# Optimization experiments

Hardware: AMD Instinct MI355X
Metric: run time of the kernel (lower is better)

## Reference

```python
import jax, jax.numpy as jnp
import numpy as np

B, S, D, F, E, K = 2, 2048, 1024, 4096, 8, 2


def setup_inputs() -> dict:
    key = jax.random.key(0)
    ks = jax.random.split(key, 6)
    s = 0.02  # init scale
    return {
        "x": jax.random.normal(ks[0], (B, S, D), dtype=jnp.float32),
        "Wr": jax.random.normal(ks[1], (D, E), dtype=jnp.float32) * s,
        "br": jnp.zeros((E,), dtype=jnp.float32),
        "W1": jax.random.normal(ks[2], (E, D, F), dtype=jnp.float32) * s,
        "b1": jnp.zeros((E, F), dtype=jnp.float32),
        "W2": jax.random.normal(ks[3], (E, F, D), dtype=jnp.float32) * s,
        "b2": jnp.zeros((E, D), dtype=jnp.float32),
        "top_k": K,
    }


def reference(x, Wr, br, W1, b1, W2, b2, top_k):
    b, s, d = x.shape
    e = Wr.shape[1]
    xt = x.reshape(-1, d)                              # [T, D], T = b*s
    logits = xt @ Wr + br                              # [T, E]
    probs = jax.nn.softmax(logits, axis=-1)            # [T, E] router probabilities
    topw, topi = jax.lax.top_k(probs, top_k)           # [T, K] each
    # combine weight per (token, expert): weight if expert in token's top-k else 0
    cw = jnp.sum(jax.nn.one_hot(topi, e, dtype=x.dtype) * topw[..., None], axis=1)  # [T, E]
    # dense grouped FFN: every expert over every token, then weighted combine
    h = jax.nn.relu(jnp.einsum('td,edf->tef', xt, W1) + b1)   # [T, E, F]
    y = jnp.einsum('tef,efd->ted', h, W2) + b2                # [T, E, D]
    out = jnp.einsum('te,ted->td', cw, y).reshape(b, s, d)    # [B, S, D]
    return out, probs.reshape(b, s, e)
```

## Files before the change

kernel.cpp:

```cpp
#include <hip/hip_runtime.h>
#include <hip/hip_bf16.h>


#define T_TOK 4096
#define D_DIM 1024
#define F_DIM 4096
#define E_NUM 8
#define CAP_ROWS 9216
#define N_TILES (CAP_ROWS/128)

typedef __attribute__((ext_vector_type(8))) short short8v;
typedef __attribute__((ext_vector_type(8))) unsigned short ushort8v;
typedef __attribute__((ext_vector_type(4))) float f32x4;

static __device__ __forceinline__ unsigned short f2bf(float f){
  union { float f; unsigned u; } v; v.f = f;
  unsigned r = (v.u + 0x7fffu + ((v.u >> 16) & 1u)) >> 16;
  return (unsigned short)r;
}
static __device__ __forceinline__ float bf2f(unsigned short s){
  union { unsigned u; float f; } v; v.u = ((unsigned)s) << 16;
  return v.f;
}

static __device__ __forceinline__ void gload16(const void* g, void* l) {
  __builtin_amdgcn_global_load_lds(
      (const __attribute__((address_space(1))) unsigned int*)g,
      (__attribute__((address_space(3))) unsigned int*)l, 16, 0, 0);
}

__global__ __launch_bounds__(256) void k_router(
    const float* __restrict__ x, const float* __restrict__ Wr,
    const float* __restrict__ br, float* __restrict__ probs_out,
    int* __restrict__ topi, float* __restrict__ topw, int* __restrict__ counts,
    unsigned short* __restrict__ xbf)
{
  const int lane = threadIdx.x & 63;
  const int t = blockIdx.x * 4 + (threadIdx.x >> 6);
  float xv[16];
  #pragma unroll
  for (int i = 0; i < 16; ++i) xv[i] = x[(size_t)t*D_DIM + i*64 + lane];
  #pragma unroll
  for (int i = 0; i < 16; ++i) xbf[(size_t)t*D_DIM + i*64 + lane] = f2bf(xv[i]);
  float pe[E_NUM];
  #pragma unroll
  for (int e = 0; e < E_NUM; ++e) {
    float p = 0.f;
    #pragma unroll
    for (int i = 0; i < 16; ++i) p += xv[i] * Wr[(i*64 + lane)*E_NUM + e];
    #pragma unroll
    for (int off = 32; off >= 1; off >>= 1) p += __shfl_xor(p, off);
    pe[e] = p + br[e];
  }
  float m = pe[0];
  #pragma unroll
  for (int e = 1; e < E_NUM; ++e) m = fmaxf(m, pe[e]);
  float s = 0.f;
  #pragma unroll
  for (int e = 0; e < E_NUM; ++e) { pe[e] = expf(pe[e] - m); s += pe[e]; }
  const float inv = 1.f / s;
  int e1 = 0; float v1 = pe[0];
  #pragma unroll
  for (int e = 1; e < E_NUM; ++e) if (pe[e] > v1) { v1 = pe[e]; e1 = e; }
  int e2 = (e1 == 0) ? 1 : 0; float v2 = pe[e2];
  #pragma unroll
  for (int e = 0; e < E_NUM; ++e) if (e != e1 && pe[e] > v2) { v2 = pe[e]; e2 = e; }
  if (lane == 0) {
    #pragma unroll
    for (int e = 0; e < E_NUM; ++e) probs_out[(size_t)t*E_NUM + e] = pe[e] * inv;
    topi[t*2+0] = e1; topw[t*2+0] = v1 * inv;
    topi[t*2+1] = e2; topw[t*2+1] = v2 * inv;
    atomicAdd(&counts[e1], 1);
    atomicAdd(&counts[e2], 1);
  }
}

__global__ __launch_bounds__(256) void k_assign(
    const int* __restrict__ counts,
    const int* __restrict__ topi, const float* __restrict__ topw,
    int* __restrict__ cursor,
    int* __restrict__ rows_token, float* __restrict__ rows_w,
    int* __restrict__ pair_of, int* __restrict__ tile_e)
{
  __shared__ int base_s[E_NUM + 1];
  if (threadIdx.x == 0) {
    int base = 0;
    #pragma unroll
    for (int e = 0; e < E_NUM; ++e) {
      base_s[e] = base;
      base += ((counts[e] + 127) >> 7) << 7;
    }
    base_s[E_NUM] = base;
  }
  __syncthreads();
  if (blockIdx.x == 0 && threadIdx.x < N_TILES) {
    const int r0 = threadIdx.x << 7;
    int e = -1;
    #pragma unroll
    for (int k = 0; k < E_NUM; ++k)
      if (r0 >= base_s[k] && r0 < base_s[k+1]) e = k;
    tile_e[threadIdx.x] = e;
  }
  const int t = blockIdx.x * 256 + threadIdx.x;
  if (t < T_TOK) {
    #pragma unroll
    for (int k = 0; k < 2; ++k) {
      const int e = topi[t*2+k];
      const int slot = atomicAdd(&cursor[e], 1);
      const int pid = base_s[e] + slot;
      rows_token[pid] = t;
      rows_w[pid] = topw[t*2+k];
      pair_of[t*2+k] = pid;
    }
  }
}

template<int R, int C>
__global__ __launch_bounds__(256) void k_tcvt(const float* __restrict__ in,
                                              unsigned short* __restrict__ out)
{
  const size_t eo = (size_t)blockIdx.z * R * C;
  const int r0 = blockIdx.y * 64, c0 = blockIdx.x * 64;
  __shared__ unsigned short ls[64][66];
  const int t = threadIdx.x;
  const int rr = t >> 4, cc = (t & 15) * 4;
  #pragma unroll
  for (int p = 0; p < 4; ++p) {
    const float4 v = *(const float4*)&in[eo + (size_t)(r0 + p*16 + rr)*C + c0 + cc];
    ls[p*16+rr][cc+0]=f2bf(v.x); ls[p*16+rr][cc+1]=f2bf(v.y);
    ls[p*16+rr][cc+2]=f2bf(v.z); ls[p*16+rr][cc+3]=f2bf(v.w);
  }
  __syncthreads();
  const int kc = (t & 7) * 8, nn0 = t >> 3;
  #pragma unroll
  for (int p = 0; p < 2; ++p) {
    const int nn = nn0 + p*32;
    ushort8v o;
    #pragma unroll
    for (int j = 0; j < 8; ++j) o[j] = ls[kc + j][nn];
    *(ushort8v*)&out[eo + (size_t)(c0 + nn)*R + r0 + kc] = o;
  }
}

template<bool GATHER, int NDIM, int KFULL, int EPI>
__global__ __launch_bounds__(256, 2) void k_gemm(
    const unsigned short* __restrict__ A,
    const unsigned short* __restrict__ Bt,
    const float* __restrict__ bias,
    const int* __restrict__ tile_e,
    const int* __restrict__ rows_token,
    const float* __restrict__ rows_w,
    unsigned short* __restrict__ outp,
    int nkt, int kch)
{
  const int tot = gridDim.x * gridDim.y;
  int flat = blockIdx.x * gridDim.y + blockIdx.y;
  flat = (flat & 7) * (tot >> 3) + (flat >> 3);
  const int bx = flat / gridDim.y;
  const int by = flat % gridDim.y;
  const int e = tile_e[by];
  if (e < 0) return;
  const int rt = by * 128;
  const int ntc = bx * 128;
  const int koff = blockIdx.z * kch;
  __shared__ __align__(16) unsigned short LB[2][256 * 64];
  const int tid = threadIdx.x;
  const int lane = tid & 63;
  const int w = tid >> 6;
  const int lr = lane >> 3;
  const int g  = (lane & 7) ^ lr;
  const unsigned short* gp[8];
  unsigned lbase[8];
  if (w < 2) {
    #pragma unroll
    for (int i = 0; i < 8; ++i) {
      const int rl = w*64 + i*8 + lr;
      const int rowidx = GATHER ? rows_token[rt + rl] : (rt + rl);
      gp[i] = A + (size_t)rowidx * KFULL + koff + g*8;
      lbase[i] = (unsigned)((w*64 + i*8) * 64);
    }
  } else {
    const unsigned short* Be = Bt + (size_t)e * NDIM * KFULL;
    #pragma unroll
    for (int i = 0; i < 8; ++i) {
      const int rl = (w-2)*64 + i*8 + lr;
      gp[i] = Be + (size_t)(ntc + rl) * KFULL + koff + g*8;
      lbase[i] = (unsigned)((128*64) + ((w-2)*64 + i*8) * 64);
    }
  }
  const int wr = w >> 1, wc = w & 1;
  const int cl = lane & 15, rgb = lane >> 4;
  const int sz = cl & 7;
  f32x4 acc[4][4] = {};

  #define STG8(tt, bb)                                          \
    { const int _ko = (tt) * 64;                                \
      _Pragma("unroll")                                         \
      for (int _i = 0; _i < 8; ++_i)                            \
        gload16(gp[_i] + _ko, &LB[bb][lbase[_i]]); }

  STG8(0, 0)
  asm volatile("s_waitcnt vmcnt(0)" ::: "memory");
  __builtin_amdgcn_s_barrier();

  for (int t = 0; t < nkt; ++t) {
    const int bb = t & 1;
    if (t + 1 < nkt) STG8(t+1, bb^1)
    const unsigned short* Sb = &LB[bb][0];
    short8v a[4][2], b[4][2];
    #pragma unroll
    for (int m = 0; m < 4; ++m) {
      a[m][0] = *(const short8v*)&Sb[(wr*64 + m*16 + cl)*64 + ((0*4+rgb)^sz)*8];
      a[m][1] = *(const short8v*)&Sb[(wr*64 + m*16 + cl)*64 + ((1*4+rgb)^sz)*8];
    }
    #pragma unroll
    for (int n = 0; n < 4; ++n) {
      b[n][0] = *(const short8v*)&Sb[(128*64) + (wc*64 + n*16 + cl)*64 + ((0*4+rgb)^sz)*8];
      b[n][1] = *(const short8v*)&Sb[(128*64) + (wc*64 + n*16 + cl)*64 + ((1*4+rgb)^sz)*8];
    }
    __builtin_amdgcn_s_setprio(1);
    #pragma unroll
    for (int m = 0; m < 4; ++m)
      #pragma unroll
      for (int n = 0; n < 4; ++n) {
        acc[m][n] = __builtin_amdgcn_mfma_f32_16x16x32_bf16(a[m][0], b[n][0], acc[m][n], 0, 0, 0);
        acc[m][n] = __builtin_amdgcn_mfma_f32_16x16x32_bf16(a[m][1], b[n][1], acc[m][n], 0, 0, 0);
      }
    __builtin_amdgcn_s_setprio(0);
    asm volatile("s_waitcnt vmcnt(0)" ::: "memory");
    __builtin_amdgcn_s_barrier();
  }
  #undef STG8

  unsigned short* op = outp;
  if (EPI == 2) op += (size_t)blockIdx.z * CAP_ROWS * NDIM;
  const bool addb = (EPI == 1) || (blockIdx.z == 0);
  const size_t ebias = (size_t)e * NDIM;
  #pragma unroll
  for (int m = 0; m < 4; ++m) {
    const int row = rt + wr*64 + m*16 + rgb*4;
    float4 rw4 = make_float4(0,0,0,0);
    if (EPI == 2) rw4 = *(const float4*)&rows_w[row];
    #pragma unroll
    for (int n = 0; n < 4; ++n) {
      const int col = ntc + wc*64 + n*16 + cl;
      const float bv = addb ? bias[ebias + col] : 0.f;
      #pragma unroll
      for (int r = 0; r < 4; ++r) {
        float v = acc[m][n][r] + bv;
        if (EPI == 1) v = fmaxf(v, 0.f);
        else          v *= ((const float*)&rw4)[r];
        const unsigned short hb = f2bf(v);
        const unsigned short ob = (unsigned short)__shfl_xor((int)(unsigned)hb, 1);
        if ((lane & 1) == 0) {
          const unsigned pk = (unsigned)hb | ((unsigned)ob << 16);
          *(unsigned*)&op[(size_t)(row + r)*NDIM + col] = pk;
        }
      }
    }
  }
}

__global__ __launch_bounds__(256) void k_combine(
    const unsigned short* __restrict__ yp, const int* __restrict__ pair_of,
    float* __restrict__ out, int ksplit)
{
  const int gid = blockIdx.x * 256 + threadIdx.x;
  const int t = gid >> 7;
  const int c = (gid & 127) * 8;
  float o[8] = {0,0,0,0,0,0,0,0};
  #pragma unroll
  for (int k = 0; k < 2; ++k) {
    const int p = pair_of[t*2+k];
    for (int s = 0; s < ksplit; ++s) {
      const ushort8v v = *(const ushort8v*)&yp[((size_t)s*CAP_ROWS + p)*D_DIM + c];
      #pragma unroll
      for (int j = 0; j < 8; ++j) o[j] += bf2f(v[j]);
    }
  }
  float4 o0; o0.x=o[0]; o0.y=o[1]; o0.z=o[2]; o0.w=o[3];
  float4 o1; o1.x=o[4]; o1.y=o[5]; o1.z=o[6]; o1.w=o[7];
  *(float4*)&out[(size_t)t*D_DIM + c]     = o0;
  *(float4*)&out[(size_t)t*D_DIM + c + 4] = o1;
}

extern "C" void kernel_launch(void* const* d_in, const int* in_sizes, int n_in,
                              void* d_out, int out_size, void* d_ws, size_t ws_size,
                              hipStream_t stream)
{
  const float* x  = (const float*)d_in[0];
  const float* Wr = (const float*)d_in[1];
  const float* br = (const float*)d_in[2];
  const float* W1 = (const float*)d_in[3];
  const float* b1 = (const float*)d_in[4];
  const float* W2 = (const float*)d_in[5];
  const float* b2 = (const float*)d_in[6];
  (void)in_sizes; (void)n_in; (void)out_size;

  float* out   = (float*)d_out;
  float* probs = out + (size_t)T_TOK * D_DIM;

  char* w = (char*)d_ws;
  size_t off = 0;
  int*   counts     = (int*)(w + off); off += 256;
  int*   cursor     = (int*)(w + off); off += 256;
  int*   rows_token = (int*)(w + off); off += (size_t)CAP_ROWS*4;
  float* rows_w     = (float*)(w + off); off += (size_t)CAP_ROWS*4;
  const size_t zbytes = off;
  int*   tile_e     = (int*)(w + off); off += 3072;
  int*   topi       = (int*)(w + off); off += (size_t)T_TOK*2*4;
  float* topw       = (float*)(w + off); off += (size_t)T_TOK*2*4;
  int*   pair_of    = (int*)(w + off); off += (size_t)T_TOK*2*4;
  off = (off + 255) & ~(size_t)255;
  unsigned short* xbf = (unsigned short*)(w + off); off += (size_t)T_TOK*D_DIM*2;
  unsigned short* Wt  = (unsigned short*)(w + off); off += (size_t)E_NUM*D_DIM*F_DIM*2;
  unsigned short* h   = (unsigned short*)(w + off); off += (size_t)CAP_ROWS*F_DIM*2;
  unsigned short* yp  = (unsigned short*)(w + off);
  const size_t ypart_bytes = (size_t)CAP_ROWS * D_DIM * 2;
  int ksplit = 1;
  if (ws_size >= off + 4 * ypart_bytes) ksplit = 4;
  else if (ws_size >= off + 2 * ypart_bytes) ksplit = 2;
  const int kch2 = F_DIM / ksplit;
  const int nkt2 = kch2 / 64;

  hipMemsetAsync(d_ws, 0, zbytes, stream);
  k_router<<<T_TOK / 4, 256, 0, stream>>>(x, Wr, br, probs, topi, topw, counts, xbf);
  k_assign<<<T_TOK / 256, 256, 0, stream>>>(counts, topi, topw, cursor,
                                            rows_token, rows_w, pair_of, tile_e);
  k_tcvt<D_DIM, F_DIM><<<dim3(F_DIM/64, D_DIM/64, E_NUM), 256, 0, stream>>>(W1, Wt);
  k_gemm<true, F_DIM, D_DIM, 1><<<dim3(F_DIM/128, N_TILES, 1), 256, 0, stream>>>(
      xbf, Wt, b1, tile_e, rows_token, rows_w, h, D_DIM/64, D_DIM);
  k_tcvt<F_DIM, D_DIM><<<dim3(D_DIM/64, F_DIM/64, E_NUM), 256, 0, stream>>>(W2, Wt);
  k_gemm<false, D_DIM, F_DIM, 2><<<dim3(D_DIM/128, N_TILES, ksplit), 256, 0, stream>>>(
      h, Wt, b2, tile_e, rows_token, rows_w, yp, nkt2, kch2);
  k_combine<<<T_TOK * D_DIM / 8 / 256, 256, 0, stream>>>(yp, pair_of, out, ksplit);
}
```

Measured before the change: 469.3 us.

## Make grouped GEMMs persistent with fixed grid and reduce FFN2 split-K to two

Both expert GEMM kernels now launch a fixed grid of 512 workgroups that loop over output tiles in an XCD-grouped order, where before there was one workgroup per tile. This skips empty capacity tiles without paying for launching them and keeps the tiles a workgroup walks through close together for L2 reuse. The second GEMM's split-K drops from up to 4 to at most 2, which cuts partial-output traffic and combine work but leaves fewer tiles to spread across the grid. The loop adds per-tile index arithmetic, and leftover tiles at the end may balance unevenly across workgroups.

```diff
diff --git a/kernel.cpp b/kernel.cpp
--- a/kernel.cpp
+++ b/kernel.cpp
@@ -8,6 +8,7 @@
 #define E_NUM 8
 #define CAP_ROWS 9216
 #define N_TILES (CAP_ROWS/128)
+#define PGRID 512
 
 typedef __attribute__((ext_vector_type(8))) short short8v;
 typedef __attribute__((ext_vector_type(8))) unsigned short ushort8v;
@@ -151,110 +152,121 @@
     const int* __restrict__ rows_token,
     const float* __restrict__ rows_w,
     unsigned short* __restrict__ outp,
-    int nkt, int kch)
-{
-  const int tot = gridDim.x * gridDim.y;
-  int flat = blockIdx.x * gridDim.y + blockIdx.y;
-  flat = (flat & 7) * (tot >> 3) + (flat >> 3);
-  const int bx = flat / gridDim.y;
-  const int by = flat % gridDim.y;
-  const int e = tile_e[by];
-  if (e < 0) return;
-  const int rt = by * 128;
-  const int ntc = bx * 128;
-  const int koff = blockIdx.z * kch;
+    int tot, int nbx, int nkt, int kch)
+{
+  const int q = blockIdx.x & 7;
+  const int bslot = blockIdx.x >> 3;
+  const int region = tot >> 3;
+  const int cpq = region / N_TILES;
   __shared__ __align__(16) unsigned short LB[2][256 * 64];
   const int tid = threadIdx.x;
   const int lane = tid & 63;
   const int w = tid >> 6;
   const int lr = lane >> 3;
   const int g  = (lane & 7) ^ lr;
-  const unsigned short* gp[8];
   unsigned lbase[8];
   if (w < 2) {
     #pragma unroll
-    for (int i = 0; i < 8; ++i) {
-      const int rl = w*64 + i*8 + lr;
-      const int rowidx = GATHER ? rows_token[rt + rl] : (rt + rl);
-      gp[i] = A + (size_t)rowidx * KFULL + koff + g*8;
-      lbase[i] = (unsigned)((w*64 + i*8) * 64);
-    }
+    for (int i = 0; i < 8; ++i) lbase[i] = (unsigned)((w*64 + i*8) * 64);
   } else {
-    const unsigned short* Be = Bt + (size_t)e * NDIM * KFULL;
-    #pragma unroll
-    for (int i = 0; i < 8; ++i) {
-      const int rl = (w-2)*64 + i*8 + lr;
-      gp[i] = Be + (size_t)(ntc + rl) * KFULL + koff + g*8;
-      lbase[i] = (unsigned)((128*64) + ((w-2)*64 + i*8) * 64);
-    }
+    #pragma unroll
+    for (int i = 0; i < 8; ++i) lbase[i] = (unsigned)((128*64) + ((w-2)*64 + i*8) * 64);
   }
   const int wr = w >> 1, wc = w & 1;
   const int cl = lane & 15, rgb = lane >> 4;
   const int sz = cl & 7;
-  f32x4 acc[4][4] = {};
-
-  #define STG8(tt, bb)                                          \
-    { const int _ko = (tt) * 64;                                \
-      _Pragma("unroll")                                         \
-      for (int _i = 0; _i < 8; ++_i)                            \
-        gload16(gp[_i] + _ko, &LB[bb][lbase[_i]]); }
-
-  STG8(0, 0)
-  asm volatile("s_waitcnt vmcnt(0)" ::: "memory");
-  __builtin_amdgcn_s_barrier();
-
-  for (int t = 0; t < nkt; ++t) {
-    const int bb = t & 1;
-    if (t + 1 < nkt) STG8(t+1, bb^1)
-    const unsigned short* Sb = &LB[bb][0];
-    short8v a[4][2], b[4][2];
-    #pragma unroll
-    for (int m = 0; m < 4; ++m) {
-      a[m][0] = *(const short8v*)&Sb[(wr*64 + m*16 + cl)*64 + ((0*4+rgb)^sz)*8];
-      a[m][1] = *(const short8v*)&Sb[(wr*64 + m*16 + cl)*64 + ((1*4+rgb)^sz)*8];
-    }
-    #pragma unroll
-    for (int n = 0; n < 4; ++n) {
-      b[n][0] = *(const short8v*)&Sb[(128*64) + (wc*64 + n*16 + cl)*64 + ((0*4+rgb)^sz)*8];
-      b[n][1] = *(const short8v*)&Sb[(128*64) + (wc*64 + n*16 + cl)*64 + ((1*4+rgb)^sz)*8];
-    }
-    __builtin_amdgcn_s_setprio(1);
-    #pragma unroll
-    for (int m = 0; m < 4; ++m)
-      #pragma unroll
-      for (int n = 0; n < 4; ++n) {
-        acc[m][n] = __builtin_amdgcn_mfma_f32_16x16x32_bf16(a[m][0], b[n][0], acc[m][n], 0, 0, 0);
-        acc[m][n] = __builtin_amdgcn_mfma_f32_16x16x32_bf16(a[m][1], b[n][1], acc[m][n], 0, 0, 0);
-      }
-    __builtin_amdgcn_s_setprio(0);
+
+  for (int tw = bslot; tw < region; tw += (PGRID >> 3)) {
+    const int combo = q * cpq + tw / N_TILES;
+    const int by = tw % N_TILES;
+    const int bx = combo % nbx;
+    const int z  = combo / nbx;
+    const int e = tile_e[by];
+    if (e < 0) continue;
+    const int rt = by * 128;
+    const int ntc = bx * 128;
+    const int koff = z * kch;
+    const unsigned short* gp[8];
+    if (w < 2) {
+      #pragma unroll
+      for (int i = 0; i < 8; ++i) {
+        const int rl = w*64 + i*8 + lr;
+        const int rowidx = GATHER ? rows_token[rt + rl] : (rt + rl);
+        gp[i] = A + (size_t)rowidx * KFULL + koff + g*8;
+      }
+    } else {
+      const unsigned short* Be = Bt + (size_t)e * NDIM * KFULL;
+      #pragma unroll
+      for (int i = 0; i < 8; ++i) {
+        const int rl = (w-2)*64 + i*8 + lr;
+        gp[i] = Be + (size_t)(ntc + rl) * KFULL + koff + g*8;
+      }
+    }
+    f32x4 acc[4][4] = {};
+
+    #define STG8(tt, bb)                                          \
+      { const int _ko = (tt) * 64;                                \
+        _Pragma("unroll")                                         \
+        for (int _i = 0; _i < 8; ++_i)                            \
+          gload16(gp[_i] + _ko, &LB[bb][lbase[_i]]); }
+
+    STG8(0, 0)
     asm volatile("s_waitcnt vmcnt(0)" ::: "memory");
     __builtin_amdgcn_s_barrier();
-  }
-  #undef STG8
-
-  unsigned short* op = outp;
-  if (EPI == 2) op += (size_t)blockIdx.z * CAP_ROWS * NDIM;
-  const bool addb = (EPI == 1) || (blockIdx.z == 0);
-  const size_t ebias = (size_t)e * NDIM;
-  #pragma unroll
-  for (int m = 0; m < 4; ++m) {
-    const int row = rt + wr*64 + m*16 + rgb*4;
-    float4 rw4 = make_float4(0,0,0,0);
-    if (EPI == 2) rw4 = *(const float4*)&rows_w[row];
-    #pragma unroll
-    for (int n = 0; n < 4; ++n) {
-      const int col = ntc + wc*64 + n*16 + cl;
-      const float bv = addb ? bias[ebias + col] : 0.f;
-      #pragma unroll
-      for (int r = 0; r < 4; ++r) {
-        float v = acc[m][n][r] + bv;
-        if (EPI == 1) v = fmaxf(v, 0.f);
-        else          v *= ((const float*)&rw4)[r];
-        const unsigned short hb = f2bf(v);
-        const unsigned short ob = (unsigned short)__shfl_xor((int)(unsigned)hb, 1);
-        if ((lane & 1) == 0) {
-          const unsigned pk = (unsigned)hb | ((unsigned)ob << 16);
-          *(unsigned*)&op[(size_t)(row + r)*NDIM + col] = pk;
+
+    for (int t = 0; t < nkt; ++t) {
+      const int bb = t & 1;
+      if (t + 1 < nkt) STG8(t+1, bb^1)
+      const unsigned short* Sb = &LB[bb][0];
+      short8v a[4][2], b[4][2];
+      #pragma unroll
+      for (int m = 0; m < 4; ++m) {
+        a[m][0] = *(const short8v*)&Sb[(wr*64 + m*16 + cl)*64 + ((0*4+rgb)^sz)*8];
+        a[m][1] = *(const short8v*)&Sb[(wr*64 + m*16 + cl)*64 + ((1*4+rgb)^sz)*8];
+      }
+      #pragma unroll
+      for (int n = 0; n < 4; ++n) {
+        b[n][0] = *(const short8v*)&Sb[(128*64) + (wc*64 + n*16 + cl)*64 + ((0*4+rgb)^sz)*8];
+        b[n][1] = *(const short8v*)&Sb[(128*64) + (wc*64 + n*16 + cl)*64 + ((1*4+rgb)^sz)*8];
+      }
+      __builtin_amdgcn_s_setprio(1);
+      #pragma unroll
+      for (int m = 0; m < 4; ++m)
+        #pragma unroll
+        for (int n = 0; n < 4; ++n) {
+          acc[m][n] = __builtin_amdgcn_mfma_f32_16x16x32_bf16(a[m][0], b[n][0], acc[m][n], 0, 0, 0);
+          acc[m][n] = __builtin_amdgcn_mfma_f32_16x16x32_bf16(a[m][1], b[n][1], acc[m][n], 0, 0, 0);
+        }
+      __builtin_amdgcn_s_setprio(0);
+      asm volatile("s_waitcnt vmcnt(0)" ::: "memory");
+      __builtin_amdgcn_s_barrier();
+    }
+    #undef STG8
+
+    unsigned short* op = outp;
+    if (EPI == 2) op += (size_t)z * CAP_ROWS * NDIM;
+    const bool addb = (EPI == 1) || (z == 0);
+    const size_t ebias = (size_t)e * NDIM;
+    #pragma unroll
+    for (int m = 0; m < 4; ++m) {
+      const int row = rt + wr*64 + m*16 + rgb*4;
+      float4 rw4 = make_float4(0,0,0,0);
+      if (EPI == 2) rw4 = *(const float4*)&rows_w[row];
+      #pragma unroll
+      for (int n = 0; n < 4; ++n) {
+        const int col = ntc + wc*64 + n*16 + cl;
+        const float bv = addb ? bias[ebias + col] : 0.f;
+        #pragma unroll
+        for (int r = 0; r < 4; ++r) {
+          float v = acc[m][n][r] + bv;
+          if (EPI == 1) v = fmaxf(v, 0.f);
+          else          v *= ((const float*)&rw4)[r];
+          const unsigned short hb = f2bf(v);
+          const unsigned short ob = (unsigned short)__shfl_xor((int)(unsigned)hb, 1);
+          if ((lane & 1) == 0) {
+            const unsigned pk = (unsigned)hb | ((unsigned)ob << 16);
+            *(unsigned*)&op[(size_t)(row + r)*NDIM + col] = pk;
+          }
         }
       }
     }
@@ -317,9 +329,7 @@
   unsigned short* h   = (unsigned short*)(w + off); off += (size_t)CAP_ROWS*F_DIM*2;
   unsigned short* yp  = (unsigned short*)(w + off);
   const size_t ypart_bytes = (size_t)CAP_ROWS * D_DIM * 2;
-  int ksplit = 1;
-  if (ws_size >= off + 4 * ypart_bytes) ksplit = 4;
-  else if (ws_size >= off + 2 * ypart_bytes) ksplit = 2;
+  const int ksplit = (ws_size >= off + 2 * ypart_bytes) ? 2 : 1;
   const int kch2 = F_DIM / ksplit;
   const int nkt2 = kch2 / 64;
 
@@ -328,10 +338,12 @@
   k_assign<<<T_TOK / 256, 256, 0, stream>>>(counts, topi, topw, cursor,
                                             rows_token, rows_w, pair_of, tile_e);
   k_tcvt<D_DIM, F_DIM><<<dim3(F_DIM/64, D_DIM/64, E_NUM), 256, 0, stream>>>(W1, Wt);
-  k_gemm<true, F_DIM, D_DIM, 1><<<dim3(F_DIM/128, N_TILES, 1), 256, 0, stream>>>(
-      xbf, Wt, b1, tile_e, rows_token, rows_w, h, D_DIM/64, D_DIM);
+  k_gemm<true, F_DIM, D_DIM, 1><<<PGRID, 256, 0, stream>>>(
+      xbf, Wt, b1, tile_e, rows_token, rows_w, h,
+      (F_DIM/128)*N_TILES, F_DIM/128, D_DIM/64, D_DIM);
   k_tcvt<F_DIM, D_DIM><<<dim3(D_DIM/64, F_DIM/64, E_NUM), 256, 0, stream>>>(W2, Wt);
-  k_gemm<false, D_DIM, F_DIM, 2><<<dim3(D_DIM/128, N_TILES, ksplit), 256, 0, stream>>>(
-      h, Wt, b2, tile_e, rows_token, rows_w, yp, nkt2, kch2);
+  k_gemm<false, D_DIM, F_DIM, 2><<<PGRID, 256, 0, stream>>>(
+      h, Wt, b2, tile_e, rows_token, rows_w, yp,
+      (D_DIM/128)*N_TILES*ksplit, D_DIM/128, nkt2, kch2);
   k_combine<<<T_TOK * D_DIM / 8 / 256, 256, 0, stream>>>(yp, pair_of, out, ksplit);
 }
```

New measurement: 452.1 us. -3.7%, faster.

## Overlap W2 transpose-convert with first expert GEMM in one fused launch

Applied to the files above, without the earlier changes.

Merges the first grouped GEMM and the W2 fp32-to-bf16 transpose into a single kernel. The leading blocks compute GEMM tiles and the trailing 1024 blocks transpose W2 into a separate buffer, so the memory-bound conversion can fill idle CUs during the GEMM tail and one launch boundary goes away. This needs an extra 64MB workspace for a second weight buffer, with a fallback to the old sequential path when the workspace is too small. The fused kernel keeps the same launch bounds and LDS size, so occupancy is unchanged, but the transpose blocks may compete with the GEMM for bandwidth.

```diff
diff --git a/kernel.cpp b/kernel.cpp
--- a/kernel.cpp
+++ b/kernel.cpp
@@ -143,7 +143,7 @@
 }
 
 template<bool GATHER, int NDIM, int KFULL, int EPI>
-__global__ __launch_bounds__(256, 2) void k_gemm(
+static __device__ __forceinline__ void gemm_tile(
     const unsigned short* __restrict__ A,
     const unsigned short* __restrict__ Bt,
     const float* __restrict__ bias,
@@ -151,19 +151,14 @@
     const int* __restrict__ rows_token,
     const float* __restrict__ rows_w,
     unsigned short* __restrict__ outp,
-    int nkt, int kch)
-{
-  const int tot = gridDim.x * gridDim.y;
-  int flat = blockIdx.x * gridDim.y + blockIdx.y;
-  flat = (flat & 7) * (tot >> 3) + (flat >> 3);
-  const int bx = flat / gridDim.y;
-  const int by = flat % gridDim.y;
+    int bx, int by, int z, int nkt, int kch,
+    unsigned short (*LB)[256*64])
+{
   const int e = tile_e[by];
   if (e < 0) return;
   const int rt = by * 128;
   const int ntc = bx * 128;
-  const int koff = blockIdx.z * kch;
-  __shared__ __align__(16) unsigned short LB[2][256 * 64];
+  const int koff = z * kch;
   const int tid = threadIdx.x;
   const int lane = tid & 63;
   const int w = tid >> 6;
@@ -233,8 +228,8 @@
   #undef STG8
 
   unsigned short* op = outp;
-  if (EPI == 2) op += (size_t)blockIdx.z * CAP_ROWS * NDIM;
-  const bool addb = (EPI == 1) || (blockIdx.z == 0);
+  if (EPI == 2) op += (size_t)z * CAP_ROWS * NDIM;
+  const bool addb = (EPI == 1) || (z == 0);
   const size_t ebias = (size_t)e * NDIM;
   #pragma unroll
   for (int m = 0; m < 4; ++m) {
@@ -261,6 +256,81 @@
   }
 }
 
+template<bool GATHER, int NDIM, int KFULL, int EPI>
+__global__ __launch_bounds__(256, 2) void k_gemm(
+    const unsigned short* __restrict__ A,
+    const unsigned short* __restrict__ Bt,
+    const float* __restrict__ bias,
+    const int* __restrict__ tile_e,
+    const int* __restrict__ rows_token,
+    const float* __restrict__ rows_w,
+    unsigned short* __restrict__ outp,
+    int nkt, int kch)
+{
+  __shared__ __align__(16) unsigned short LB[2][256 * 64];
+  const int tot = gridDim.x * gridDim.y;
+  int flat = blockIdx.x * gridDim.y + blockIdx.y;
+  flat = (flat & 7) * (tot >> 3) + (flat >> 3);
+  gemm_tile<GATHER, NDIM, KFULL, EPI>(A, Bt, bias, tile_e, rows_token, rows_w,
+                                      outp, flat / gridDim.y, flat % gridDim.y,
+                                      blockIdx.z, nkt, kch, LB);
+}
+
+__global__ __launch_bounds__(256, 2) void k_fused1(
+    const unsigned short* __restrict__ xbf,
+    const unsigned short* __restrict__ W1t,
+    const float* __restrict__ b1,
+    const int* __restrict__ tile_e,
+    const int* __restrict__ rows_token,
+    const float* __restrict__ rows_w,
+    unsigned short* __restrict__ h,
+    const float* __restrict__ W2,
+    unsigned short* __restrict__ W2t)
+{
+  __shared__ __align__(16) unsigned short LB[2][256 * 64];
+  constexpr int NG = (F_DIM/128) * N_TILES;
+  const int b = blockIdx.x;
+  if (b < NG) {
+    const int x = b & 31;
+    const int y = b >> 5;
+    int flat = x * N_TILES + y;
+    flat = (flat & 7) * (NG >> 3) + (flat >> 3);
+    gemm_tile<true, F_DIM, D_DIM, 1>(xbf, W1t, b1, tile_e, rows_token, rows_w,
+                                     h, flat / N_TILES, flat % N_TILES, 0,
+                                     D_DIM/64, D_DIM, LB);
+  } else {
+    auto ls = (unsigned short (*)[66])(&LB[0][0]);
+    const int tb = b - NG;
+    const int e = tb >> 7;
+    const int rem = tb & 127;
+    const int c0 = (rem & 15) * 64;
+    const int rg = (rem >> 4) * 512;
+    const size_t eo = (size_t)e * F_DIM * D_DIM;
+    const int t = threadIdx.x;
+    const int rr = t >> 4, cc = (t & 15) * 4;
+    const int kc = (t & 7) * 8, nn0 = t >> 3;
+    for (int s = 0; s < 8; ++s) {
+      const int r0 = rg + s * 64;
+      #pragma unroll
+      for (int p = 0; p < 4; ++p) {
+        const float4 v = *(const float4*)&W2[eo + (size_t)(r0 + p*16 + rr)*D_DIM + c0 + cc];
+        ls[p*16+rr][cc+0]=f2bf(v.x); ls[p*16+rr][cc+1]=f2bf(v.y);
+        ls[p*16+rr][cc+2]=f2bf(v.z); ls[p*16+rr][cc+3]=f2bf(v.w);
+      }
+      __syncthreads();
+      #pragma unroll
+      for (int p = 0; p < 2; ++p) {
+        const int nn = nn0 + p*32;
+        ushort8v o;
+        #pragma unroll
+        for (int j = 0; j < 8; ++j) o[j] = ls[kc + j][nn];
+        *(ushort8v*)&W2t[eo + (size_t)(c0 + nn)*F_DIM + r0 + kc] = o;
+      }
+      __syncthreads();
+    }
+  }
+}
+
 __global__ __launch_bounds__(256) void k_combine(
     const unsigned short* __restrict__ yp, const int* __restrict__ pair_of,
     float* __restrict__ out, int ksplit)
@@ -313,13 +383,29 @@
   int*   pair_of    = (int*)(w + off); off += (size_t)T_TOK*2*4;
   off = (off + 255) & ~(size_t)255;
   unsigned short* xbf = (unsigned short*)(w + off); off += (size_t)T_TOK*D_DIM*2;
-  unsigned short* Wt  = (unsigned short*)(w + off); off += (size_t)E_NUM*D_DIM*F_DIM*2;
-  unsigned short* h   = (unsigned short*)(w + off); off += (size_t)CAP_ROWS*F_DIM*2;
-  unsigned short* yp  = (unsigned short*)(w + off);
-  const size_t ypart_bytes = (size_t)CAP_ROWS * D_DIM * 2;
-  int ksplit = 1;
-  if (ws_size >= off + 4 * ypart_bytes) ksplit = 4;
-  else if (ws_size >= off + 2 * ypart_bytes) ksplit = 2;
+  unsigned short* W1t = (unsigned short*)(w + off); off += (size_t)E_NUM*D_DIM*F_DIM*2;
+
+  const size_t WT = (size_t)E_NUM*D_DIM*F_DIM*2;
+  const size_t HB = (size_t)CAP_ROWS*F_DIM*2;
+  const size_t YP = (size_t)CAP_ROWS*D_DIM*2;
+
+  bool fused; int ksplit;
+  if      (ws_size >= off + WT + HB + 4*YP) { fused = true;  ksplit = 4; }
+  else if (ws_size >= off + WT + HB + 2*YP) { fused = true;  ksplit = 2; }
+  else if (ws_size >= off + HB + 4*YP)      { fused = false; ksplit = 4; }
+  else if (ws_size >= off + HB + 2*YP)      { fused = false; ksplit = 2; }
+  else                                      { fused = false; ksplit = 1; }
+
+  unsigned short* W2t;
+  unsigned short* h;
+  if (fused) {
+    W2t = (unsigned short*)(w + off); off += WT;
+    h   = (unsigned short*)(w + off); off += HB;
+  } else {
+    W2t = W1t;
+    h   = (unsigned short*)(w + off); off += HB;
+  }
+  unsigned short* yp = (unsigned short*)(w + off);
   const int kch2 = F_DIM / ksplit;
   const int nkt2 = kch2 / 64;
 
@@ -327,11 +413,17 @@
   k_router<<<T_TOK / 4, 256, 0, stream>>>(x, Wr, br, probs, topi, topw, counts, xbf);
   k_assign<<<T_TOK / 256, 256, 0, stream>>>(counts, topi, topw, cursor,
                                             rows_token, rows_w, pair_of, tile_e);
-  k_tcvt<D_DIM, F_DIM><<<dim3(F_DIM/64, D_DIM/64, E_NUM), 256, 0, stream>>>(W1, Wt);
-  k_gemm<true, F_DIM, D_DIM, 1><<<dim3(F_DIM/128, N_TILES, 1), 256, 0, stream>>>(
-      xbf, Wt, b1, tile_e, rows_token, rows_w, h, D_DIM/64, D_DIM);
-  k_tcvt<F_DIM, D_DIM><<<dim3(D_DIM/64, F_DIM/64, E_NUM), 256, 0, stream>>>(W2, Wt);
+  k_tcvt<D_DIM, F_DIM><<<dim3(F_DIM/64, D_DIM/64, E_NUM), 256, 0, stream>>>(W1, W1t);
+
+  if (fused) {
+    k_fused1<<<(F_DIM/128)*N_TILES + 1024, 256, 0, stream>>>(
+        xbf, W1t, b1, tile_e, rows_token, rows_w, h, W2, W2t);
+  } else {
+    k_gemm<true, F_DIM, D_DIM, 1><<<dim3(F_DIM/128, N_TILES), 256, 0, stream>>>(
+        xbf, W1t, b1, tile_e, rows_token, rows_w, h, D_DIM/64, D_DIM);
+    k_tcvt<F_DIM, D_DIM><<<dim3(D_DIM/64, F_DIM/64, E_NUM), 256, 0, stream>>>(W2, W2t);
+  }
   k_gemm<false, D_DIM, F_DIM, 2><<<dim3(D_DIM/128, N_TILES, ksplit), 256, 0, stream>>>(
-      h, Wt, b2, tile_e, rows_token, rows_w, yp, nkt2, kch2);
+      h, W2t, b2, tile_e, rows_token, rows_w, yp, nkt2, kch2);
   k_combine<<<T_TOK * D_DIM / 8 / 256, 256, 0, stream>>>(yp, pair_of, out, ksplit);
 }
```

New measurement: 461.0 us. No clear change (-1.8%).
